# Performance work log

Measured on AMD Instinct MI355X. Metric: run time of the kernel, lower is better.

Reference implementation:

```python
import jax, jax.numpy as jnp
import numpy as np

H = 5  # hidden size of both LSTMs

def _lstm_layer(x, Wih, Whh, bih, bhh):
    """x: [B,T,I] -> hs: [B,T,H]. PyTorch gate order i,f,g,o; zero init state."""
    B, T, _ = x.shape
    # precompute input contribution for all timesteps: [T,B,4H]
    xg = (jnp.einsum('bti,gi->btg', x, Wih) + bih + bhh).transpose(1, 0, 2)
    def step(carry, xg_t):
        h, c = carry
        g = xg_t + h @ Whh.T
        i, f, gg, o = jnp.split(g, 4, axis=-1)
        c = jax.nn.sigmoid(f) * c + jax.nn.sigmoid(i) * jnp.tanh(gg)
        h = jax.nn.sigmoid(o) * jnp.tanh(c)
        return (h, c), h
    h0 = jnp.zeros((B, H), x.dtype)
    (_, _), hs = jax.lax.scan(step, (h0, h0), xg)
    return hs.transpose(1, 0, 2)  # [B,T,H]

def setup_inputs() -> dict:
    key = jax.random.key(0)
    ks = jax.random.split(key, 32)
    B, T = 16384, 128
    def u(k, shape, fan):
        s = 1.0 / np.sqrt(fan)
        return jax.random.uniform(k, shape, jnp.float32, -s, s)
    inp = {
        'x1': jax.random.normal(ks[0], (B, T, 5), jnp.float32),
        'x2': jax.random.normal(ks[1], (B, T, 5), jnp.float32),
        # lstm1 (1 layer)
        'Wih1': u(ks[2], (4*H, 5), H), 'Whh1': u(ks[3], (4*H, H), H),
        'bih1': u(ks[4], (4*H,), H), 'bhh1': u(ks[5], (4*H,), H),
        # lstm2 layer 0
        'Wih2a': u(ks[6], (4*H, 5), H), 'Whh2a': u(ks[7], (4*H, H), H),
        'bih2a': u(ks[8], (4*H,), H), 'bhh2a': u(ks[9], (4*H,), H),
        # lstm2 layer 1
        'Wih2b': u(ks[10], (4*H, H), H), 'Whh2b': u(ks[11], (4*H, H), H),
        'bih2b': u(ks[12], (4*H,), H), 'bhh2b': u(ks[13], (4*H,), H),
        # FC stack 20->32->32->16->16->5
        'W1': u(ks[14], (32, 20), 20), 'b1': u(ks[15], (32,), 20),
        'W2': u(ks[16], (32, 32), 32), 'b2': u(ks[17], (32,), 32),
        'W3': u(ks[18], (16, 32), 32), 'b3': u(ks[19], (16,), 32),
        'W4': u(ks[20], (16, 16), 16), 'b4': u(ks[21], (16,), 16),
        'W5': u(ks[22], (5, 16), 16), 'b5': u(ks[23], (5,), 16),
    }
    return inp

def reference(x1, x2, Wih1, Whh1, bih1, bhh1, Wih2a, Whh2a, bih2a, bhh2a,
              Wih2b, Whh2b, bih2b, bhh2b, W1, b1, W2, b2, W3, b3, W4, b4, W5, b5):
    out1 = _lstm_layer(x1, Wih1, Whh1, bih1, bhh1)[:, -1, :]            # [B,5]
    h2 = _lstm_layer(x2, Wih2a, Whh2a, bih2a, bhh2a)                    # [B,T,5]
    out2 = _lstm_layer(h2, Wih2b, Whh2b, bih2b, bhh2b)[:, -1, :]        # [B,5]
    out = jnp.concatenate([x1[:, -1, :], x2[:, -1, :], out1, out2], axis=1)  # [B,20]
    out = jax.nn.relu(out @ W1.T + b1)
    out = jax.nn.relu(out @ W2.T + b2)
    out = jax.nn.relu(out @ W3.T + b3)
    out = jax.nn.relu(out @ W4.T + b4)
    return out @ W5.T + b5  # [B,5]
```

## Files before the change

kernel.cpp:

```cpp
#include <hip/hip_runtime.h>

#define DEV __device__ __forceinline__

DEV float fexp2(float x) { return __builtin_amdgcn_exp2f(x); }
DEV float frcp(float x) { return __builtin_amdgcn_rcpf(x); }

template <int S>
DEV float qbcast(float x) {
  int i = __float_as_int(x);
  i = __builtin_amdgcn_update_dpp(0, i, S * 0x55, 0xF, 0xF, true);
  return __int_as_float(i);
}

DEV float bperm(int byte_addr, float x) {
  return __int_as_float(
      __builtin_amdgcn_ds_bpermute(byte_addr, __float_as_int(x)));
}

struct Cell {
  float wih[5][5];
  float whh[5][5];
  float b[5];
};

DEV void load_cell(Cell& W, const float* __restrict__ Wih,
                   const float* __restrict__ Whh, const float* __restrict__ bih,
                   const float* __restrict__ bhh, int s) {
#pragma unroll
  for (int j = 0; j < 5; ++j) {
    int r = 5 * s + j;
#pragma unroll
    for (int k = 0; k < 5; ++k) {
      W.wih[j][k] = Wih[r * 5 + k];
      W.whh[j][k] = Whh[r * 5 + k];
    }
    W.b[j] = bih[r] + bhh[r];
  }
}

DEV void cell_step(const Cell& W, float kexp, float m2, float a2,
                   const float x[5], float h[5], float c[5]) {
  float a[5];
#pragma unroll
  for (int j = 0; j < 5; ++j) {
    float acc = W.b[j];
#pragma unroll
    for (int k = 0; k < 5; ++k) acc = fmaf(W.wih[j][k], x[k], acc);
#pragma unroll
    for (int k = 0; k < 5; ++k) acc = fmaf(W.whh[j][k], h[k], acc);
    float e = fexp2(acc * kexp);
    float r = frcp(1.0f + e);
    a[j] = fmaf(m2, r, a2);
  }
#pragma unroll
  for (int j = 0; j < 5; ++j) {
    float I = qbcast<0>(a[j]);
    float F = qbcast<1>(a[j]);
    float G = qbcast<2>(a[j]);
    float O = qbcast<3>(a[j]);
    float cj = fmaf(F, c[j], I * G);
    c[j] = cj;
    float e2 = fexp2(cj * -2.885390082f);
    float tc = fmaf(2.0f, frcp(1.0f + e2), -1.0f);
    h[j] = O * tc;
  }
}

__global__ __launch_bounds__(64, 4) void rnn_pipe_kernel(
    const float* __restrict__ x1, const float* __restrict__ x2,
    const float* __restrict__ Wih1, const float* __restrict__ Whh1,
    const float* __restrict__ bih1, const float* __restrict__ bhh1,
    const float* __restrict__ Wih2a, const float* __restrict__ Whh2a,
    const float* __restrict__ bih2a, const float* __restrict__ bhh2a,
    const float* __restrict__ Wih2b, const float* __restrict__ Whh2b,
    const float* __restrict__ bih2b, const float* __restrict__ bhh2b,
    const float* __restrict__ W1, const float* __restrict__ b1,
    const float* __restrict__ W2, const float* __restrict__ b2,
    const float* __restrict__ W3, const float* __restrict__ b3,
    const float* __restrict__ W4, const float* __restrict__ b4,
    const float* __restrict__ W5, const float* __restrict__ b5,
    float* __restrict__ out, int B) {
  __shared__ float sIn[5][20];
  __shared__ float sA[5][32];
  __shared__ float sB[5][32];

  const int lane = threadIdx.x;
  const int q = lane >> 2;
  const int s = lane & 3;

  if (q < 15) {
    const int e_w = q / 3;
    const int cell = q - e_w * 3;
    const int eg = blockIdx.x * 5 + e_w;
    const int egc = (eg < B) ? eg : (B - 1);
    const bool c2 = (cell == 2);
    const float* xbase = (cell == 1) ? x2 : x1;
    const float* px = xbase + (size_t)egc * 640;

    Cell W;
    if (cell == 0)
      load_cell(W, Wih1, Whh1, bih1, bhh1, s);
    else if (cell == 1)
      load_cell(W, Wih2a, Whh2a, bih2a, bhh2a, s);
    else
      load_cell(W, Wih2b, Whh2b, bih2b, bhh2b, s);

    const float kexp = (s == 2) ? -2.885390082f : -1.442695041f;
    const float m2 = (s == 2) ? 2.0f : 1.0f;
    const float a2 = (s == 2) ? -1.0f : 0.0f;
    const int bpaddr = ((c2 ? lane - 4 : lane) << 2);

    float h[5], c[5], hp[5], xcur[5];
#pragma unroll
    for (int k = 0; k < 5; ++k) {
      h[k] = c[k] = hp[k] = 0.0f;
      xcur[k] = px[k];
    }

    for (int t = 0; t < 128; ++t) {
      const int tn = (t < 127) ? t + 1 : 127;
      float xn[5];
#pragma unroll
      for (int k = 0; k < 5; ++k) xn[k] = px[tn * 5 + k];
      float xin[5];
#pragma unroll
      for (int k = 0; k < 5; ++k) xin[k] = c2 ? hp[k] : xcur[k];
      cell_step(W, kexp, m2, a2, xin, h, c);
      if (t == 0 && c2) {
#pragma unroll
        for (int k = 0; k < 5; ++k) {
          h[k] = 0.0f;
          c[k] = 0.0f;
        }
      }
#pragma unroll
      for (int k = 0; k < 5; ++k) hp[k] = bperm(bpaddr, h[k]);
#pragma unroll
      for (int k = 0; k < 5; ++k) xcur[k] = xn[k];
    }
    if (c2) {
      float xin[5];
#pragma unroll
      for (int k = 0; k < 5; ++k) xin[k] = hp[k];
      cell_step(W, kexp, m2, a2, xin, h, c);
    }

    if (eg < B && s == 0) {
      if (cell == 0) {
#pragma unroll
        for (int k = 0; k < 5; ++k) {
          sIn[e_w][k] = xcur[k];
          sIn[e_w][10 + k] = h[k];
        }
      } else if (cell == 1) {
#pragma unroll
        for (int k = 0; k < 5; ++k) sIn[e_w][5 + k] = xcur[k];
      } else {
#pragma unroll
        for (int k = 0; k < 5; ++k) sIn[e_w][15 + k] = h[k];
      }
    }
  }
  __syncthreads();

  for (int task = lane; task < 160; task += 64) {
    int e = task >> 5, n = task & 31;
    float acc = b1[n];
#pragma unroll
    for (int k = 0; k < 20; ++k) acc = fmaf(W1[n * 20 + k], sIn[e][k], acc);
    sA[e][n] = fmaxf(acc, 0.0f);
  }
  __syncthreads();
  for (int task = lane; task < 160; task += 64) {
    int e = task >> 5, n = task & 31;
    float acc = b2[n];
#pragma unroll
    for (int k = 0; k < 32; ++k) acc = fmaf(W2[n * 32 + k], sA[e][k], acc);
    sB[e][n] = fmaxf(acc, 0.0f);
  }
  __syncthreads();
  for (int task = lane; task < 80; task += 64) {
    int e = task >> 4, n = task & 15;
    float acc = b3[n];
#pragma unroll
    for (int k = 0; k < 32; ++k) acc = fmaf(W3[n * 32 + k], sB[e][k], acc);
    sA[e][n] = fmaxf(acc, 0.0f);
  }
  __syncthreads();
  for (int task = lane; task < 80; task += 64) {
    int e = task >> 4, n = task & 15;
    float acc = b4[n];
#pragma unroll
    for (int k = 0; k < 16; ++k) acc = fmaf(W4[n * 16 + k], sA[e][k], acc);
    sB[e][n] = fmaxf(acc, 0.0f);
  }
  __syncthreads();
  for (int task = lane; task < 25; task += 64) {
    int e = task / 5, n = task - 5 * (task / 5);
    float acc = b5[n];
#pragma unroll
    for (int k = 0; k < 16; ++k) acc = fmaf(W5[n * 16 + k], sB[e][k], acc);
    int eg = blockIdx.x * 5 + e;
    if (eg < B) out[(size_t)eg * 5 + n] = acc;
  }
}

extern "C" void kernel_launch(void* const* d_in, const int* in_sizes, int n_in,
                              void* d_out, int out_size, void* d_ws,
                              size_t ws_size, hipStream_t stream) {
  const float* x1 = (const float*)d_in[0];
  const float* x2 = (const float*)d_in[1];
  const float* Wih1 = (const float*)d_in[2];
  const float* Whh1 = (const float*)d_in[3];
  const float* bih1 = (const float*)d_in[4];
  const float* bhh1 = (const float*)d_in[5];
  const float* Wih2a = (const float*)d_in[6];
  const float* Whh2a = (const float*)d_in[7];
  const float* bih2a = (const float*)d_in[8];
  const float* bhh2a = (const float*)d_in[9];
  const float* Wih2b = (const float*)d_in[10];
  const float* Whh2b = (const float*)d_in[11];
  const float* bih2b = (const float*)d_in[12];
  const float* bhh2b = (const float*)d_in[13];
  const float* W1 = (const float*)d_in[14];
  const float* b1 = (const float*)d_in[15];
  const float* W2 = (const float*)d_in[16];
  const float* b2 = (const float*)d_in[17];
  const float* W3 = (const float*)d_in[18];
  const float* b3 = (const float*)d_in[19];
  const float* W4 = (const float*)d_in[20];
  const float* b4 = (const float*)d_in[21];
  const float* W5 = (const float*)d_in[22];
  const float* b5 = (const float*)d_in[23];

  int B = in_sizes[0] / 640;
  int blocks = (B + 4) / 5;

  rnn_pipe_kernel<<<blocks, 64, 0, stream>>>(
      x1, x2, Wih1, Whh1, bih1, bhh1, Wih2a, Whh2a, bih2a, bhh2a, Wih2b, Whh2b,
      bih2b, bhh2b, W1, b1, W2, b2, W3, b3, W4, b4, W5, b5, (float*)d_out, B);
}
```

Before: 271.3 us.

## Remap LSTM lanes to one hidden unit per lane, all three cells per lane

```diff
diff --git a/kernel.cpp b/kernel.cpp
--- a/kernel.cpp
+++ b/kernel.cpp
@@ -1,72 +1,61 @@
 #include <hip/hip_runtime.h>
 
 #define DEV __device__ __forceinline__
+#define KSIG (-1.442695041f)
+#define KTANH (-2.885390082f)
 
 DEV float fexp2(float x) { return __builtin_amdgcn_exp2f(x); }
 DEV float frcp(float x) { return __builtin_amdgcn_rcpf(x); }
-
-template <int S>
-DEV float qbcast(float x) {
-  int i = __float_as_int(x);
-  i = __builtin_amdgcn_update_dpp(0, i, S * 0x55, 0xF, 0xF, true);
-  return __int_as_float(i);
-}
-
-DEV float bperm(int byte_addr, float x) {
-  return __int_as_float(
-      __builtin_amdgcn_ds_bpermute(byte_addr, __float_as_int(x)));
-}
-
-struct Cell {
-  float wih[5][5];
-  float whh[5][5];
-  float b[5];
+DEV float bperm(int a, float x) {
+  return __int_as_float(__builtin_amdgcn_ds_bpermute(a, __float_as_int(x)));
+}
+
+struct CellB {
+  float w[4][10];
+  float b[4];
 };
 
-DEV void load_cell(Cell& W, const float* __restrict__ Wih,
-                   const float* __restrict__ Whh, const float* __restrict__ bih,
-                   const float* __restrict__ bhh, int s) {
-#pragma unroll
-  for (int j = 0; j < 5; ++j) {
-    int r = 5 * s + j;
+DEV void load_cellB(CellB& W, int u, const float* __restrict__ Wih,
+                    const float* __restrict__ Whh,
+                    const float* __restrict__ bih,
+                    const float* __restrict__ bhh) {
+#pragma unroll
+  for (int rt = 0; rt < 4; ++rt) {
+    int row = 5 * rt + u;
+    float kx = (rt == 2) ? KTANH : KSIG;
 #pragma unroll
     for (int k = 0; k < 5; ++k) {
-      W.wih[j][k] = Wih[r * 5 + k];
-      W.whh[j][k] = Whh[r * 5 + k];
+      W.w[rt][k] = kx * Wih[row * 5 + k];
+      W.w[rt][5 + k] = kx * Whh[row * 5 + k];
     }
-    W.b[j] = bih[r] + bhh[r];
-  }
-}
-
-DEV void cell_step(const Cell& W, float kexp, float m2, float a2,
-                   const float x[5], float h[5], float c[5]) {
-  float a[5];
-#pragma unroll
-  for (int j = 0; j < 5; ++j) {
-    float acc = W.b[j];
-#pragma unroll
-    for (int k = 0; k < 5; ++k) acc = fmaf(W.wih[j][k], x[k], acc);
-#pragma unroll
-    for (int k = 0; k < 5; ++k) acc = fmaf(W.whh[j][k], h[k], acc);
-    float e = fexp2(acc * kexp);
-    float r = frcp(1.0f + e);
-    a[j] = fmaf(m2, r, a2);
-  }
-#pragma unroll
-  for (int j = 0; j < 5; ++j) {
-    float I = qbcast<0>(a[j]);
-    float F = qbcast<1>(a[j]);
-    float G = qbcast<2>(a[j]);
-    float O = qbcast<3>(a[j]);
-    float cj = fmaf(F, c[j], I * G);
-    c[j] = cj;
-    float e2 = fexp2(cj * -2.885390082f);
-    float tc = fmaf(2.0f, frcp(1.0f + e2), -1.0f);
-    h[j] = O * tc;
-  }
-}
-
-__global__ __launch_bounds__(64, 4) void rnn_pipe_kernel(
+    W.b[rt] = kx * (bih[row] + bhh[row]);
+  }
+}
+
+DEV void cellB_step(const CellB& W, const float xin[5], float hAll[5],
+                    float& c, const int bp[5]) {
+  float acc[4];
+#pragma unroll
+  for (int rt = 0; rt < 4; ++rt) {
+    float a = W.b[rt];
+#pragma unroll
+    for (int k = 0; k < 5; ++k) a = fmaf(W.w[rt][k], xin[k], a);
+#pragma unroll
+    for (int k = 0; k < 5; ++k) a = fmaf(W.w[rt][5 + k], hAll[k], a);
+    acc[rt] = a;
+  }
+  float gi = frcp(1.f + fexp2(acc[0]));
+  float gf = frcp(1.f + fexp2(acc[1]));
+  float gg = fmaf(2.f, frcp(1.f + fexp2(acc[2])), -1.f);
+  float go = frcp(1.f + fexp2(acc[3]));
+  c = fmaf(gf, c, gi * gg);
+  float th = fmaf(2.f, frcp(1.f + fexp2(KTANH * c)), -1.f);
+  float h = go * th;
+#pragma unroll
+  for (int u2 = 0; u2 < 5; ++u2) hAll[u2] = bperm(bp[u2], h);
+}
+
+__global__ __launch_bounds__(64, 2) void rnn5_kernel(
     const float* __restrict__ x1, const float* __restrict__ x2,
     const float* __restrict__ Wih1, const float* __restrict__ Whh1,
     const float* __restrict__ bih1, const float* __restrict__ bhh1,
@@ -80,128 +69,105 @@
     const float* __restrict__ W4, const float* __restrict__ b4,
     const float* __restrict__ W5, const float* __restrict__ b5,
     float* __restrict__ out, int B) {
-  __shared__ float sIn[5][20];
-  __shared__ float sA[5][32];
-  __shared__ float sB[5][32];
-
-  const int lane = threadIdx.x;
-  const int q = lane >> 2;
-  const int s = lane & 3;
-
-  if (q < 15) {
-    const int e_w = q / 3;
-    const int cell = q - e_w * 3;
-    const int eg = blockIdx.x * 5 + e_w;
-    const int egc = (eg < B) ? eg : (B - 1);
-    const bool c2 = (cell == 2);
-    const float* xbase = (cell == 1) ? x2 : x1;
-    const float* px = xbase + (size_t)egc * 640;
-
-    Cell W;
-    if (cell == 0)
-      load_cell(W, Wih1, Whh1, bih1, bhh1, s);
-    else if (cell == 1)
-      load_cell(W, Wih2a, Whh2a, bih2a, bhh2a, s);
-    else
-      load_cell(W, Wih2b, Whh2b, bih2b, bhh2b, s);
-
-    const float kexp = (s == 2) ? -2.885390082f : -1.442695041f;
-    const float m2 = (s == 2) ? 2.0f : 1.0f;
-    const float a2 = (s == 2) ? -1.0f : 0.0f;
-    const int bpaddr = ((c2 ? lane - 4 : lane) << 2);
-
-    float h[5], c[5], hp[5], xcur[5];
+  __shared__ float sIn[12][20];
+  __shared__ float sA[12][32];
+  __shared__ float sB[12][32];
+
+  const int l = threadIdx.x;
+  const int g = l / 5;
+  const int u = l - 5 * g;
+  const bool act = (g < 12);
+  const int el = act ? g : 11;
+  const int eg = blockIdx.x * 12 + el;
+  const int egc = (eg < B) ? eg : (B - 1);
+
+  CellB Wc0, Wc1, Wc2;
+  load_cellB(Wc0, u, Wih1, Whh1, bih1, bhh1);
+  load_cellB(Wc1, u, Wih2a, Whh2a, bih2a, bhh2a);
+  load_cellB(Wc2, u, Wih2b, Whh2b, bih2b, bhh2b);
+
+  int bp[5];
+#pragma unroll
+  for (int u2 = 0; u2 < 5; ++u2) bp[u2] = (5 * g + u2) * 4;
+
+  const float* px1 = x1 + (size_t)egc * 640;
+  const float* px2 = x2 + (size_t)egc * 640;
+
+  float h1[5], h2a[5], h2b[5];
+  float c1 = 0.f, c2 = 0.f, c3 = 0.f;
+  float xa[5], xb[5];
+#pragma unroll
+  for (int k = 0; k < 5; ++k) {
+    h1[k] = h2a[k] = h2b[k] = 0.f;
+    xa[k] = px1[k];
+    xb[k] = px2[k];
+  }
+
+  for (int t = 0; t < 128; ++t) {
+    const int tn = (t < 127) ? t + 1 : 127;
+    float na[5], nb[5];
 #pragma unroll
     for (int k = 0; k < 5; ++k) {
-      h[k] = c[k] = hp[k] = 0.0f;
-      xcur[k] = px[k];
+      na[k] = px1[tn * 5 + k];
+      nb[k] = px2[tn * 5 + k];
     }
-
-    for (int t = 0; t < 128; ++t) {
-      const int tn = (t < 127) ? t + 1 : 127;
-      float xn[5];
-#pragma unroll
-      for (int k = 0; k < 5; ++k) xn[k] = px[tn * 5 + k];
-      float xin[5];
-#pragma unroll
-      for (int k = 0; k < 5; ++k) xin[k] = c2 ? hp[k] : xcur[k];
-      cell_step(W, kexp, m2, a2, xin, h, c);
-      if (t == 0 && c2) {
-#pragma unroll
-        for (int k = 0; k < 5; ++k) {
-          h[k] = 0.0f;
-          c[k] = 0.0f;
-        }
-      }
-#pragma unroll
-      for (int k = 0; k < 5; ++k) hp[k] = bperm(bpaddr, h[k]);
-#pragma unroll
-      for (int k = 0; k < 5; ++k) xcur[k] = xn[k];
+    cellB_step(Wc0, xa, h1, c1, bp);
+    cellB_step(Wc1, xb, h2a, c2, bp);
+    cellB_step(Wc2, h2a, h2b, c3, bp);
+#pragma unroll
+    for (int k = 0; k < 5; ++k) {
+      xa[k] = na[k];
+      xb[k] = nb[k];
     }
-    if (c2) {
-      float xin[5];
-#pragma unroll
-      for (int k = 0; k < 5; ++k) xin[k] = hp[k];
-      cell_step(W, kexp, m2, a2, xin, h, c);
-    }
-
-    if (eg < B && s == 0) {
-      if (cell == 0) {
-#pragma unroll
-        for (int k = 0; k < 5; ++k) {
-          sIn[e_w][k] = xcur[k];
-          sIn[e_w][10 + k] = h[k];
-        }
-      } else if (cell == 1) {
-#pragma unroll
-        for (int k = 0; k < 5; ++k) sIn[e_w][5 + k] = xcur[k];
-      } else {
-#pragma unroll
-        for (int k = 0; k < 5; ++k) sIn[e_w][15 + k] = h[k];
-      }
-    }
-  }
-  __syncthreads();
-
-  for (int task = lane; task < 160; task += 64) {
+  }
+
+  if (act) {
+    sIn[el][u] = xa[u];
+    sIn[el][5 + u] = xb[u];
+    sIn[el][10 + u] = h1[u];
+    sIn[el][15 + u] = h2b[u];
+  }
+  __syncthreads();
+
+  for (int task = l; task < 12 * 32; task += 64) {
     int e = task >> 5, n = task & 31;
     float acc = b1[n];
 #pragma unroll
     for (int k = 0; k < 20; ++k) acc = fmaf(W1[n * 20 + k], sIn[e][k], acc);
-    sA[e][n] = fmaxf(acc, 0.0f);
-  }
-  __syncthreads();
-  for (int task = lane; task < 160; task += 64) {
+    sA[e][n] = fmaxf(acc, 0.f);
+  }
+  __syncthreads();
+  for (int task = l; task < 12 * 32; task += 64) {
     int e = task >> 5, n = task & 31;
     float acc = b2[n];
 #pragma unroll
     for (int k = 0; k < 32; ++k) acc = fmaf(W2[n * 32 + k], sA[e][k], acc);
-    sB[e][n] = fmaxf(acc, 0.0f);
-  }
-  __syncthreads();
-  for (int task = lane; task < 80; task += 64) {
+    sB[e][n] = fmaxf(acc, 0.f);
+  }
+  __syncthreads();
+  for (int task = l; task < 12 * 16; task += 64) {
     int e = task >> 4, n = task & 15;
     float acc = b3[n];
 #pragma unroll
     for (int k = 0; k < 32; ++k) acc = fmaf(W3[n * 32 + k], sB[e][k], acc);
-    sA[e][n] = fmaxf(acc, 0.0f);
-  }
-  __syncthreads();
-  for (int task = lane; task < 80; task += 64) {
+    sA[e][n] = fmaxf(acc, 0.f);
+  }
+  __syncthreads();
+  for (int task = l; task < 12 * 16; task += 64) {
     int e = task >> 4, n = task & 15;
     float acc = b4[n];
 #pragma unroll
     for (int k = 0; k < 16; ++k) acc = fmaf(W4[n * 16 + k], sA[e][k], acc);
-    sB[e][n] = fmaxf(acc, 0.0f);
-  }
-  __syncthreads();
-  for (int task = lane; task < 25; task += 64) {
-    int e = task / 5, n = task - 5 * (task / 5);
+    sB[e][n] = fmaxf(acc, 0.f);
+  }
+  __syncthreads();
+  if (l < 60) {
+    int e = l / 5, n = l - 5 * (l / 5);
     float acc = b5[n];
 #pragma unroll
     for (int k = 0; k < 16; ++k) acc = fmaf(W5[n * 16 + k], sB[e][k], acc);
-    int eg = blockIdx.x * 5 + e;
-    if (eg < B) out[(size_t)eg * 5 + n] = acc;
+    int ego = blockIdx.x * 12 + e;
+    if (ego < B) out[(size_t)ego * 5 + n] = acc;
   }
 }
 
@@ -234,9 +200,9 @@
   const float* b5 = (const float*)d_in[23];
 
   int B = in_sizes[0] / 640;
-  int blocks = (B + 4) / 5;
-
-  rnn_pipe_kernel<<<blocks, 64, 0, stream>>>(
+  int blocks = (B + 11) / 12;
+
+  rnn5_kernel<<<blocks, 64, 0, stream>>>(
       x1, x2, Wih1, Whh1, bih1, bhh1, Wih2a, Whh2a, bih2a, bhh2a, Wih2b, Whh2b,
       bih2b, bhh2b, W1, b1, W2, b2, W3, b3, W4, b4, W5, b5, (float*)d_out, B);
 }
```

New measurement: 241.9 us. -10.8%, faster.
